# Kernel optimization log

Hardware: AMD Instinct MI355X
Metric: run time of the kernel (lower is better)

Reference implementation:

```python
import jax, jax.numpy as jnp
import numpy as np

# RWKV6Attention config (fla): expand_k=expand_v=0.5, proj_low_rank_dim=64, gate_low_rank_dim=64
H = 2048          # hidden_size
NH = 16           # num heads
KD = H // 2       # key_dim = hidden * expand_k
VD = H // 2       # value_dim = hidden * expand_v
DK = KD // NH     # head_qk_dim = 64
DV = VD // NH     # head_v_dim = 64
RLOW = 64         # proj_low_rank_dim
GLOW = 64         # gate_low_rank_dim
EPS = 1e-5
B, T = 2, 1024


def setup_inputs() -> dict:
    key = jax.random.key(0)
    ks = jax.random.split(key, 18)

    def rn(k, shape, scale=0.02):
        return (jax.random.normal(k, shape) * scale).astype(jnp.float32)

    return {
        "x": jax.random.normal(ks[0], (B, T, H), dtype=jnp.float32),
        "mu_x": rn(ks[1], (H,), 0.5),            # LerpLinear mixing coeff
        "Wx1": rn(ks[2], (H, 5 * RLOW)),          # x_proj[0].linear (hidden -> 5*r)
        "Wx2": rn(ks[3], (H, 5, RLOW)),           # x_proj[2].weight viewed [hidden, 5, r]
        "x_bias": rn(ks[4], (5, H)),
        "Wr": rn(ks[5], (H, KD)),
        "Wk": rn(ks[6], (H, KD)),
        "Wv": rn(ks[7], (H, VD)),
        "Ww_a": rn(ks[8], (H, GLOW)),             # w_proj LoRA down
        "Ww_b": rn(ks[9], (GLOW, KD)),            # w_proj LoRA up
        "bw": rn(ks[10], (KD,)),
        "Wg_a": rn(ks[11], (H, GLOW)),            # g_proj LoRA down
        "Wg_b": rn(ks[12], (GLOW, VD)),           # g_proj LoRA up
        "bg": rn(ks[13], (VD,)),
        "bonus": rn(ks[14], (NH, DK), 0.5),       # per-head bonus u
        "ln_w": jnp.ones((DV,), jnp.float32),     # FusedLayerNormSwishGate affine
        "ln_b": jnp.zeros((DV,), jnp.float32),
        "Wo": rn(ks[15], (VD, H)),
    }


def reference(x, mu_x, Wx1, Wx2, x_bias, Wr, Wk, Wv, Ww_a, Ww_b, bw,
              Wg_a, Wg_b, bg, bonus, ln_w, ln_b, Wo):
    b, t, _ = x.shape
    # time_shift: zero-pad one step at front, drop last
    shifted = jnp.pad(x, ((0, 0), (1, 0), (0, 0)))[:, :t]
    delta = shifted - x

    # low-rank data-dependent lerp coefficients for r, w, k, v, g
    lr = jnp.tanh(((x + delta * mu_x) @ Wx1).reshape(b, t, 5, RLOW))
    mus = jnp.einsum('btnr,hnr->btnh', lr, Wx2) + x_bias  # [B,T,5,H]
    mr, mw, mk, mv, mg = (mus[:, :, i] for i in range(5))

    r = (x + delta * mr) @ Wr                                   # [B,T,KD]
    w = jnp.tanh((x + delta * mw) @ Ww_a) @ Ww_b + bw           # [B,T,KD]
    k = (x + delta * mk) @ Wk                                   # [B,T,KD]
    v = (x + delta * mv) @ Wv                                   # [B,T,VD]
    g = jnp.tanh((x + delta * mg) @ Wg_a) @ Wg_b + bg           # [B,T,VD]

    r = r.reshape(b, t, NH, DK)
    k = k.reshape(b, t, NH, DK)
    v = v.reshape(b, t, NH, DV)
    decay = jnp.exp(-jnp.exp(w.reshape(b, t, NH, DK)))          # w = -exp(w); decay = exp(w)

    # linear-attention recurrence: o_t = r_t . (S + u * k_t v_t^T); S <- decay_t * S + k_t v_t^T
    xs = (jnp.moveaxis(r, 1, 0), jnp.moveaxis(k, 1, 0),
          jnp.moveaxis(v, 1, 0), jnp.moveaxis(decay, 1, 0))
    S0 = jnp.zeros((b, NH, DK, DV), x.dtype)

    def step(S, inp):
        rt, kt, vt, dt = inp
        kv = kt[..., :, None] * vt[..., None, :]                # [B,NH,DK,DV]
        ot = jnp.einsum('bhk,bhkv->bhv', rt, S + bonus[None, :, :, None] * kv)
        S = dt[..., None] * S + kv
        return S, ot

    _, o = jax.lax.scan(step, S0, xs)                           # o: [T,B,NH,DV]
    o = jnp.moveaxis(o, 0, 1)                                   # [B,T,NH,DV]

    # per-head layernorm + swish gate
    g = g.reshape(b, t, NH, DV)
    mean = o.mean(-1, keepdims=True)
    var = o.var(-1, keepdims=True)
    on = (o - mean) * jax.lax.rsqrt(var + EPS) * ln_w + ln_b
    o = on * g * jax.nn.sigmoid(g)

    return o.reshape(b, t, VD) @ Wo
```

## Files before the change

### kernel.cpp

```cpp
#include <hip/hip_runtime.h>
#include <hip/hip_bf16.h>

#define H_    2048
#define NH_   16
#define KD_   1024
#define DK_   64
#define T_    1024
#define B_    2
#define M_    (B_*T_)
#define RL_   64
#define CC_   32
#define NC_   (T_/CC_)

typedef short bf16x8 __attribute__((ext_vector_type(8)));
typedef float f32x4  __attribute__((ext_vector_type(4)));

__device__ __forceinline__ ushort bf16r(float f) {
    union { float f; unsigned u; } v; v.f = f;
    return (ushort)((v.u + 0x7FFF + ((v.u >> 16) & 1)) >> 16);
}

__device__ __forceinline__ void gl_lds16(const void* g, void* l) {
    __builtin_amdgcn_global_load_lds((const __attribute__((address_space(1))) void*)g,
                                     (__attribute__((address_space(3))) void*)l, 16, 0, 0);
}


__global__ __launch_bounds__(256) void mix_mu_t(const float* __restrict__ x,
                                                const float* __restrict__ mu,
                                                ushort* __restrict__ At) {
    int c = blockIdx.x * 256 + threadIdx.x;
    int bt = c >> 8, k8 = c & 255;
    int k = k8 << 3;
    int t = bt & (T_ - 1);
    const float* xp = &x[(size_t)bt * H_ + k];
    float4 xa = *(const float4*)xp;
    float4 xb = *(const float4*)(xp + 4);
    float4 sa = make_float4(0,0,0,0), sb = make_float4(0,0,0,0);
    if (t > 0) { sa = *(const float4*)(xp - H_); sb = *(const float4*)(xp - H_ + 4); }
    float4 ma = *(const float4*)&mu[k];
    float4 mb = *(const float4*)&mu[k + 4];
    ushort o[8];
    o[0] = bf16r(xa.x + (sa.x - xa.x) * ma.x);
    o[1] = bf16r(xa.y + (sa.y - xa.y) * ma.y);
    o[2] = bf16r(xa.z + (sa.z - xa.z) * ma.z);
    o[3] = bf16r(xa.w + (sa.w - xa.w) * ma.w);
    o[4] = bf16r(xb.x + (sb.x - xb.x) * mb.x);
    o[5] = bf16r(xb.y + (sb.y - xb.y) * mb.y);
    o[6] = bf16r(xb.z + (sb.z - xb.z) * mb.z);
    o[7] = bf16r(xb.w + (sb.w - xb.w) * mb.w);
    int rb = bt >> 7, kb = k8 >> 2, g = k8 & 3, r = bt & 127;
    *(uint4*)&At[(((size_t)(rb * 64 + kb)) << 12) + ((g << 7) + r) * 8] = *(uint4*)o;
}

__global__ __launch_bounds__(256) void convert_w(const float* __restrict__ W,
                                                 ushort* __restrict__ Wt,
                                                 int K, int N) {
    __shared__ float s[32][68];
    int kb = blockIdx.y, nb = blockIdx.x;
    int t = threadIdx.x;
    #pragma unroll
    for (int i = 0; i < 2; ++i) {
        int q = t + i * 256;
        int k = q >> 4, c4 = (q & 15) << 2;
        *(float4*)&s[k][c4] = *(const float4*)&W[(size_t)(kb * 32 + k) * N + nb * 64 + c4];
    }
    __syncthreads();
    int g = t >> 6, c = t & 63;
    ushort o[8];
    #pragma unroll
    for (int e = 0; e < 8; ++e) o[e] = bf16r(s[g * 8 + e][c]);
    *(uint4*)&Wt[((size_t)(nb * (K >> 5) + kb)) * 2048 + t * 8] = *(uint4*)o;
}

__global__ __launch_bounds__(256) void convert_w3(const float* __restrict__ W0,
                                                  const float* __restrict__ W1,
                                                  const float* __restrict__ W2,
                                                  ushort* __restrict__ Wt) {
    __shared__ float s[32][68];
    int z = blockIdx.z;
    const float* W = (z == 0) ? W0 : (z == 1) ? W1 : W2;
    ushort* dst = Wt + (size_t)z * ((size_t)H_ * KD_);
    int kb = blockIdx.y, nb = blockIdx.x;
    int t = threadIdx.x;
    #pragma unroll
    for (int i = 0; i < 2; ++i) {
        int q = t + i * 256;
        int k = q >> 4, c4 = (q & 15) << 2;
        *(float4*)&s[k][c4] = *(const float4*)&W[(size_t)(kb * 32 + k) * KD_ + nb * 64 + c4];
    }
    __syncthreads();
    int g = t >> 6, c = t & 63;
    ushort o[8];
    #pragma unroll
    for (int e = 0; e < 8; ++e) o[e] = bf16r(s[g * 8 + e][c]);
    *(uint4*)&dst[((size_t)(nb * (H_ >> 5) + kb)) * 2048 + t * 8] = *(uint4*)o;
}

template<int EPI, int NB>
__global__ __launch_bounds__(256) void gemm_bf16t(const ushort* __restrict__ A0,
                                                  const ushort* __restrict__ A1,
                                                  const ushort* __restrict__ A2,
                                                  const ushort* __restrict__ Bt0,
                                                  float* __restrict__ C0,
                                                  int K, int ldc) {
    __shared__ ushort Alds[2][4096];
    __shared__ ushort Blds[2][2048];
    int tid = threadIdx.x;
    int w = tid >> 6, l = tid & 63;
    int KB = K >> 5;
    int z = (NB > 1) ? blockIdx.z : 0;
    const ushort* At = (NB > 1) ? (z == 0 ? A0 : z == 1 ? A1 : A2) : A0;
    const ushort* Bt = Bt0 + (size_t)z * ((size_t)H_ * KD_);
    float* C = C0 + (size_t)z * ((size_t)M_ * KD_);
    const ushort* Ag = At + (size_t)blockIdx.y * KB * 4096 + tid * 8;
    const ushort* Bg = Bt + (size_t)blockIdx.x * KB * 2048 + tid * 8;
    int wr = (w >> 1) << 6, wc = (w & 1) << 5;
    int a_off = (((l >> 4) << 7) + wr + (l & 15)) << 3;
    int b_off = (((l >> 4) << 6) + wc + (l & 15)) << 3;
    f32x4 acc[8] = {};
    gl_lds16(Ag,        &Alds[0][w * 512]);
    gl_lds16(Ag + 2048, &Alds[0][w * 512 + 2048]);
    gl_lds16(Bg,        &Blds[0][w * 512]);
    __syncthreads();
    for (int kt = 0; kt < KB; ++kt) {
        int cur = kt & 1;
        if (kt + 1 < KB) {
            Ag += 4096; Bg += 2048;
            int nxt = cur ^ 1;
            gl_lds16(Ag,        &Alds[nxt][w * 512]);
            gl_lds16(Ag + 2048, &Alds[nxt][w * 512 + 2048]);
            gl_lds16(Bg,        &Blds[nxt][w * 512]);
        }
        bf16x8 af0 = *(const bf16x8*)&Alds[cur][a_off];
        bf16x8 af1 = *(const bf16x8*)&Alds[cur][a_off + 128];
        bf16x8 af2 = *(const bf16x8*)&Alds[cur][a_off + 256];
        bf16x8 af3 = *(const bf16x8*)&Alds[cur][a_off + 384];
        bf16x8 bf0 = *(const bf16x8*)&Blds[cur][b_off];
        bf16x8 bf1 = *(const bf16x8*)&Blds[cur][b_off + 128];
        acc[0] = __builtin_amdgcn_mfma_f32_16x16x32_bf16(af0, bf0, acc[0], 0, 0, 0);
        acc[1] = __builtin_amdgcn_mfma_f32_16x16x32_bf16(af0, bf1, acc[1], 0, 0, 0);
        acc[2] = __builtin_amdgcn_mfma_f32_16x16x32_bf16(af1, bf0, acc[2], 0, 0, 0);
        acc[3] = __builtin_amdgcn_mfma_f32_16x16x32_bf16(af1, bf1, acc[3], 0, 0, 0);
        acc[4] = __builtin_amdgcn_mfma_f32_16x16x32_bf16(af2, bf0, acc[4], 0, 0, 0);
        acc[5] = __builtin_amdgcn_mfma_f32_16x16x32_bf16(af2, bf1, acc[5], 0, 0, 0);
        acc[6] = __builtin_amdgcn_mfma_f32_16x16x32_bf16(af3, bf0, acc[6], 0, 0, 0);
        acc[7] = __builtin_amdgcn_mfma_f32_16x16x32_bf16(af3, bf1, acc[7], 0, 0, 0);
        __syncthreads();
    }
    int row0 = (blockIdx.y << 7) + wr + ((l >> 4) << 2);
    int col0 = (blockIdx.x << 6) + wc + (l & 15);
    #pragma unroll
    for (int fr = 0; fr < 4; ++fr)
        #pragma unroll
        for (int fc = 0; fc < 2; ++fc) {
            f32x4 v = acc[fr * 2 + fc];
            #pragma unroll
            for (int q = 0; q < 4; ++q) {
                float o = v[q];
                if (EPI == 1) o = tanhf(o);
                C[(size_t)(row0 + fr * 16 + q) * ldc + col0 + fc * 16] = o;
            }
        }
}

__global__ __launch_bounds__(256) void musgemm5_kernel(const float* __restrict__ x,
                                                       const float* __restrict__ lr,
                                                       const float* __restrict__ Wx2,
                                                       const float* __restrict__ xbias,
                                                       ushort* __restrict__ xmt_r,
                                                       float*  __restrict__ xm_w,
                                                       ushort* __restrict__ xmt_k,
                                                       ushort* __restrict__ xmt_v,
                                                       float*  __restrict__ xm_g) {
    __shared__ float sLT[64][68];
    __shared__ float sWT[64][68];
    int tid = threadIdx.x;
    int tx = tid & 15, ty = tid >> 4;
    int col0 = blockIdx.x * 64;
    int row0 = blockIdx.y * 64;
    int kcol = col0 + (tx << 2);
    int lrow = tid >> 2;
    int lk   = (tid & 3) << 2;
    #pragma unroll
    for (int b = 0; b < 5; ++b) {
        __syncthreads();
        #pragma unroll
        for (int pass = 0; pass < 4; ++pass) {
            int kk = lk + pass * 16;
            float4 lv = *(const float4*)&lr[(size_t)(row0 + lrow) * 320 + b * 64 + kk];
            float4 wv = *(const float4*)&Wx2[(size_t)(col0 + lrow) * 320 + b * 64 + kk];
            sLT[kk + 0][lrow] = lv.x; sLT[kk + 1][lrow] = lv.y;
            sLT[kk + 2][lrow] = lv.z; sLT[kk + 3][lrow] = lv.w;
            sWT[kk + 0][lrow] = wv.x; sWT[kk + 1][lrow] = wv.y;
            sWT[kk + 2][lrow] = wv.z; sWT[kk + 3][lrow] = wv.w;
        }
        __syncthreads();
        float acc[4][4] = {};
        #pragma unroll 4
        for (int k = 0; k < 64; ++k) {
            float4 a = *(const float4*)&sLT[k][ty << 2];
            float4 bb = *(const float4*)&sWT[k][tx << 2];
            float aa[4] = {a.x, a.y, a.z, a.w};
            float bv_[4] = {bb.x, bb.y, bb.z, bb.w};
            #pragma unroll
            for (int i = 0; i < 4; ++i)
                #pragma unroll
                for (int j = 0; j < 4; ++j)
                    acc[i][j] = fmaf(aa[i], bv_[j], acc[i][j]);
        }
        float4 bias4 = *(const float4*)&xbias[b * H_ + kcol];
        float bv[4] = {bias4.x, bias4.y, bias4.z, bias4.w};
        #pragma unroll
        for (int i = 0; i < 4; ++i) {
            int r = row0 + (ty << 2) + i;
            int t = r & (T_ - 1);
            const float* xrow = &x[(size_t)r * H_ + kcol];
            float4 xv = *(const float4*)xrow;
            float4 sh = make_float4(0.f, 0.f, 0.f, 0.f);
            if (t > 0) sh = *(const float4*)(xrow - H_);
            float o0 = xv.x + (sh.x - xv.x) * (acc[i][0] + bv[0]);
            float o1 = xv.y + (sh.y - xv.y) * (acc[i][1] + bv[1]);
            float o2 = xv.z + (sh.z - xv.z) * (acc[i][2] + bv[2]);
            float o3 = xv.w + (sh.w - xv.w) * (acc[i][3] + bv[3]);
            if (b == 0 || b == 2 || b == 3) {
                ushort* dst = (b == 0) ? xmt_r : (b == 2) ? xmt_k : xmt_v;
                int rb = r >> 7, kb = kcol >> 5, g = (kcol >> 3) & 3, hf = (kcol >> 2) & 1;
                ushort4 pk; pk.x = bf16r(o0); pk.y = bf16r(o1); pk.z = bf16r(o2); pk.w = bf16r(o3);
                *(ushort4*)&dst[(((size_t)(rb * 64 + kb)) << 12) + ((g << 7) + (r & 127)) * 8 + hf * 4] = pk;
            } else {
                float* dst = (b == 1) ? xm_w : xm_g;
                float4 o; o.x = o0; o.y = o1; o.z = o2; o.w = o3;
                *(float4*)&dst[(size_t)r * H_ + kcol] = o;
            }
        }
    }
}

__global__ __launch_bounds__(256) void gemm_f32_up2(const float* __restrict__ hidw,
                                                    const float* __restrict__ hidg,
                                                    const float* __restrict__ Wwb,
                                                    const float* __restrict__ Wgb,
                                                    const float* __restrict__ bw,
                                                    const float* __restrict__ bg,
                                                    float* __restrict__ db,
                                                    float* __restrict__ gb) {
    __shared__ float As[16][68];
    __shared__ float Bs[16][68];
    int z = blockIdx.z;
    const float* A = z ? hidg : hidw;
    const float* W = z ? Wgb : Wwb;
    const float* bias = z ? bg : bw;
    float* C = z ? gb : db;
    int tid = threadIdx.x;
    int tx = tid & 15, ty = tid >> 4;
    int row0 = blockIdx.y * 64, col0 = blockIdx.x * 64;
    int am = tid >> 2, ak = (tid & 3) << 2;
    int bk = tid >> 4, bn = (tid & 15) << 2;
    float acc[4][4] = {};
    float4 av = *(const float4*)&A[(size_t)(row0 + am) * 64 + ak];
    float4 bv = *(const float4*)&W[(size_t)bk * KD_ + col0 + bn];
    for (int k0 = 0; k0 < 64; k0 += 16) {
        __syncthreads();
        As[ak + 0][am] = av.x; As[ak + 1][am] = av.y;
        As[ak + 2][am] = av.z; As[ak + 3][am] = av.w;
        *(float4*)&Bs[bk][bn] = bv;
        __syncthreads();
        if (k0 + 16 < 64) {
            av = *(const float4*)&A[(size_t)(row0 + am) * 64 + k0 + 16 + ak];
            bv = *(const float4*)&W[(size_t)(k0 + 16 + bk) * KD_ + col0 + bn];
        }
        #pragma unroll
        for (int kk = 0; kk < 16; ++kk) {
            float4 a = *(const float4*)&As[kk][ty << 2];
            float4 b = *(const float4*)&Bs[kk][tx << 2];
            float aa[4] = {a.x, a.y, a.z, a.w};
            float bb[4] = {b.x, b.y, b.z, b.w};
            #pragma unroll
            for (int i = 0; i < 4; ++i)
                #pragma unroll
                for (int j = 0; j < 4; ++j)
                    acc[i][j] = fmaf(aa[i], bb[j], acc[i][j]);
        }
    }
    #pragma unroll
    for (int i = 0; i < 4; ++i) {
        int r = row0 + (ty << 2) + i;
        #pragma unroll
        for (int j = 0; j < 4; ++j) {
            int c = col0 + (tx << 2) + j;
            float v = acc[i][j] + bias[c];
            if (z == 0) v = -expf(v);
            C[(size_t)r * KD_ + c] = v;
        }
    }
}

__global__ __launch_bounds__(256) void gemm_f32_splitk2(const float* __restrict__ Aw,
                                                        const float* __restrict__ Ag2,
                                                        const float* __restrict__ Wwa,
                                                        const float* __restrict__ Wga,
                                                        float* __restrict__ partw,
                                                        float* __restrict__ partg) {
    __shared__ float As[16][68];
    __shared__ float Bs[16][68];
    int z = blockIdx.z;
    const float* A = z ? Ag2 : Aw;
    const float* W = z ? Wga : Wwa;
    float* part = z ? partg : partw;
    int tid = threadIdx.x;
    int tx = tid & 15, ty = tid >> 4;
    int row0 = blockIdx.y * 64;
    int kbase = blockIdx.x * 256;
    int am = tid >> 2, ak = (tid & 3) << 2;
    int bk = tid >> 4, bn = (tid & 15) << 2;
    float acc[4][4] = {};
    float4 av = *(const float4*)&A[(size_t)(row0 + am) * H_ + kbase + ak];
    float4 bv = *(const float4*)&W[(size_t)(kbase + bk) * 64 + bn];
    for (int k0 = 0; k0 < 256; k0 += 16) {
        __syncthreads();
        As[ak + 0][am] = av.x; As[ak + 1][am] = av.y;
        As[ak + 2][am] = av.z; As[ak + 3][am] = av.w;
        *(float4*)&Bs[bk][bn] = bv;
        __syncthreads();
        if (k0 + 16 < 256) {
            av = *(const float4*)&A[(size_t)(row0 + am) * H_ + kbase + k0 + 16 + ak];
            bv = *(const float4*)&W[(size_t)(kbase + k0 + 16 + bk) * 64 + bn];
        }
        #pragma unroll
        for (int kk = 0; kk < 16; ++kk) {
            float4 a = *(const float4*)&As[kk][ty << 2];
            float4 b = *(const float4*)&Bs[kk][tx << 2];
            float aa[4] = {a.x, a.y, a.z, a.w};
            float bb[4] = {b.x, b.y, b.z, b.w};
            #pragma unroll
            for (int i = 0; i < 4; ++i)
                #pragma unroll
                for (int j = 0; j < 4; ++j)
                    acc[i][j] = fmaf(aa[i], bb[j], acc[i][j]);
        }
    }
    float* pc = part + (size_t)blockIdx.x * (M_ * 64);
    #pragma unroll
    for (int i = 0; i < 4; ++i) {
        int r = row0 + (ty << 2) + i;
        #pragma unroll
        for (int j = 0; j < 4; ++j)
            pc[(size_t)r * 64 + (tx << 2) + j] = acc[i][j];
    }
}

__global__ __launch_bounds__(256) void reduce_tanh2(const float* __restrict__ partw,
                                                    const float* __restrict__ partg,
                                                    float* __restrict__ hidw,
                                                    float* __restrict__ hidg) {
    int z = blockIdx.y;
    const float4* p = (const float4*)(z ? partg : partw);
    float* hid = z ? hidg : hidw;
    int i = blockIdx.x * 256 + threadIdx.x;
    float4 s = p[i];
    #pragma unroll
    for (int kc = 1; kc < 8; ++kc) {
        float4 v = p[i + kc * 32768];
        s.x += v.x; s.y += v.y; s.z += v.z; s.w += v.w;
    }
    s.x = tanhf(s.x); s.y = tanhf(s.y); s.z = tanhf(s.z); s.w = tanhf(s.w);
    ((float4*)hid)[i] = s;
}

__global__ __launch_bounds__(256) void scan_chunkA(const float* r, const float* k,
                                                   const float* v, const float* ld,
                                                   const float* u,
                                                   float* rt, float* ointra,
                                                   float* Bc, float* Dc) {
    __shared__ float sR[CC_][68], sK[CC_][68], sV[CC_][68], sW[CC_][68];
    __shared__ float wc[CC_ + 1][64];
    __shared__ float sA[CC_][36];
    __shared__ float diag[CC_];
    __shared__ float sU[64];
    int bid = blockIdx.x;
    int bh = bid >> 5, c = bid & (NC_ - 1);
    int b = bh >> 4, h = bh & 15;
    int tid = threadIdx.x;
    size_t base = ((size_t)(b * T_ + c * CC_)) * KD_ + h * 64;

    for (int q = tid; q < CC_ * 16; q += 256) {
        int row = q >> 4, col4 = (q & 15) << 2;
        size_t gi = base + (size_t)row * KD_ + col4;
        *(float4*)&sR[row][col4] = *(const float4*)&r[gi];
        *(float4*)&sK[row][col4] = *(const float4*)&k[gi];
        *(float4*)&sV[row][col4] = *(const float4*)&v[gi];
        *(float4*)&sW[row][col4] = *(const float4*)&ld[gi];
    }
    if (tid < 64) sU[tid] = u[h * 64 + tid];
    __syncthreads();

    if (tid < 64) {
        float acc = 0.f;
        wc[0][tid] = 0.f;
        #pragma unroll
        for (int s = 0; s < CC_; ++s) { acc += sW[s][tid]; wc[s + 1][tid] = acc; }
    }
    {
        int tau = tid >> 3, g = tid & 7;
        float p = 0.f;
        #pragma unroll
        for (int q = 0; q < 8; ++q) {
            int i = g * 8 + q;
            p += sR[tau][i] * sU[i] * sK[tau][i];
        }
        p += __shfl_xor(p, 1, 64); p += __shfl_xor(p, 2, 64); p += __shfl_xor(p, 4, 64);
        if (g == 0) diag[tau] = p;
    }
    __syncthreads();

    for (int q = tid; q < CC_ * 64; q += 256) {
        int s = q >> 6, i = q & 63;
        float wcs  = wc[s][i];
        float wcs1 = wc[s + 1][i];
        float wcc  = wc[CC_][i];
        float rt_ = sR[s][i] * expf(wcs);
        float kt_ = sK[s][i] * expf(-wcs1);
        float bb  = sK[s][i] * expf(wcc - wcs1);
        sR[s][i] = rt_;
        sW[s][i] = kt_;
        sK[s][i] = bb;
        rt[base + (size_t)s * KD_ + i] = rt_;
    }
    if (tid < 64) Dc[(size_t)bid * 64 + tid] = expf(wc[CC_][tid]);
    __syncthreads();

    {
        int tau = tid >> 3, s0 = (tid & 7) * 4;
        float a0 = 0, a1 = 0, a2 = 0, a3 = 0;
        for (int i0 = 0; i0 < 64; i0 += 4) {
            int i = (i0 + s0) & 63;
            float4 rr = *(const float4*)&sR[tau][i];
            float4 k0v = *(const float4*)&sW[s0 + 0][i];
            float4 k1v = *(const float4*)&sW[s0 + 1][i];
            float4 k2v = *(const float4*)&sW[s0 + 2][i];
            float4 k3v = *(const float4*)&sW[s0 + 3][i];
            a0 += rr.x * k0v.x + rr.y * k0v.y + rr.z * k0v.z + rr.w * k0v.w;
            a1 += rr.x * k1v.x + rr.y * k1v.y + rr.z * k1v.z + rr.w * k1v.w;
            a2 += rr.x * k2v.x + rr.y * k2v.y + rr.z * k2v.z + rr.w * k2v.w;
            a3 += rr.x * k3v.x + rr.y * k3v.y + rr.z * k3v.z + rr.w * k3v.w;
        }
        sA[tau][s0 + 0] = (s0 + 0 < tau) ? a0 : ((s0 + 0 == tau) ? diag[tau] : 0.f);
        sA[tau][s0 + 1] = (s0 + 1 < tau) ? a1 : ((s0 + 1 == tau) ? diag[tau] : 0.f);
        sA[tau][s0 + 2] = (s0 + 2 < tau) ? a2 : ((s0 + 2 == tau) ? diag[tau] : 0.f);
        sA[tau][s0 + 3] = (s0 + 3 < tau) ? a3 : ((s0 + 3 == tau) ? diag[tau] : 0.f);
    }
    __syncthreads();

    {
        int tau = tid >> 3, j0 = (tid & 7) * 8;
        float o_[8] __attribute__((aligned(16))) = {};
        for (int s = 0; s < CC_; ++s) {
            float a = sA[tau][s];
            #pragma unroll
            for (int q = 0; q < 8; ++q) o_[q] += a * sV[s][j0 + q];
        }
        size_t ob = base + (size_t)tau * KD_ + j0;
        *(float4*)&ointra[ob]     = *(float4*)&o_[0];
        *(float4*)&ointra[ob + 4] = *(float4*)&o_[4];
    }
    {
        int i = tid >> 2, j0 = (tid & 3) * 16;
        float bacc[16] __attribute__((aligned(16))) = {};
        for (int s = 0; s < CC_; ++s) {
            float bi = sK[s][i];
            #pragma unroll
            for (int q = 0; q < 16; ++q) bacc[q] += bi * sV[s][j0 + q];
        }
        size_t bb = ((size_t)bid << 12) + i * 64 + j0;
        *(float4*)&Bc[bb + 0]  = *(float4*)&bacc[0];
        *(float4*)&Bc[bb + 4]  = *(float4*)&bacc[4];
        *(float4*)&Bc[bb + 8]  = *(float4*)&bacc[8];
        *(float4*)&Bc[bb + 12] = *(float4*)&bacc[12];
    }
}

__global__ __launch_bounds__(256) void scan_chunkB(float* BS, const float* __restrict__ Dc) {
    int g = blockIdx.x * 256 + threadIdx.x;
    int bh = g >> 12, ij = g & 4095, i = ij >> 6;
    float S = 0.f;
    size_t base = ((size_t)bh << 17) + ij;
    float bv = BS[base];
    float d  = Dc[(size_t)(bh * NC_) * 64 + i];
    for (int c = 0; c < NC_; ++c) {
        size_t idx = base + ((size_t)c << 12);
        float bv2 = 0.f, d2 = 0.f;
        if (c + 1 < NC_) {
            bv2 = BS[idx + 4096];
            d2  = Dc[(size_t)(bh * NC_ + c + 1) * 64 + i];
        }
        BS[idx] = S;
        S = d * S + bv;
        bv = bv2; d = d2;
    }
}

__global__ __launch_bounds__(256) void scan_chunkC_ln(const float* __restrict__ rt,
                                                      const float* __restrict__ BS,
                                                      const float* __restrict__ oi,
                                                      const float* __restrict__ gb,
                                                      const float* __restrict__ lw,
                                                      const float* __restrict__ lb,
                                                      ushort* __restrict__ outt) {
    __shared__ float sS[64][64];
    __shared__ float sRt[CC_][68];
    int bid = blockIdx.x;
    int bh = bid >> 5, c = bid & (NC_ - 1);
    int b = bh >> 4, h = bh & 15;
    int tid = threadIdx.x;
    size_t sbase = ((size_t)bid) << 12;
    for (int q = tid; q < 1024; q += 256)
        *(float4*)&sS[q >> 4][(q & 15) << 2] = *(const float4*)&BS[sbase + (q << 2)];
    size_t base = ((size_t)(b * T_ + c * CC_)) * KD_ + h * 64;
    for (int q = tid; q < CC_ * 16; q += 256) {
        int row = q >> 4, col4 = (q & 15) << 2;
        *(float4*)&sRt[row][col4] = *(const float4*)&rt[base + (size_t)row * KD_ + col4];
    }
    __syncthreads();
    int tau = tid >> 3, j0 = (tid & 7) * 8;
    size_t obase = base + (size_t)tau * KD_ + j0;
    float acc[8] __attribute__((aligned(16)));
    *(float4*)&acc[0] = *(const float4*)&oi[obase];
    *(float4*)&acc[4] = *(const float4*)&oi[obase + 4];
    for (int i = 0; i < 64; ++i) {
        float a = sRt[tau][i];
        #pragma unroll
        for (int q = 0; q < 8; ++q) acc[q] += a * sS[i][j0 + q];
    }
    float s = 0.f;
    #pragma unroll
    for (int q = 0; q < 8; ++q) s += acc[q];
    s += __shfl_xor(s, 1, 64); s += __shfl_xor(s, 2, 64); s += __shfl_xor(s, 4, 64);
    float mean = s * (1.f / 64.f);
    float s2 = 0.f;
    #pragma unroll
    for (int q = 0; q < 8; ++q) { float dx = acc[q] - mean; s2 += dx * dx; }
    s2 += __shfl_xor(s2, 1, 64); s2 += __shfl_xor(s2, 2, 64); s2 += __shfl_xor(s2, 4, 64);
    float inv = rsqrtf(s2 * (1.f / 64.f) + 1e-5f);
    float4 lw0 = *(const float4*)&lw[j0], lw1 = *(const float4*)&lw[j0 + 4];
    float4 lb0 = *(const float4*)&lb[j0], lb1 = *(const float4*)&lb[j0 + 4];
    float lwv[8] = {lw0.x, lw0.y, lw0.z, lw0.w, lw1.x, lw1.y, lw1.z, lw1.w};
    float lbv[8] = {lb0.x, lb0.y, lb0.z, lb0.w, lb1.x, lb1.y, lb1.z, lb1.w};
    float4 gv0 = *(const float4*)&gb[obase], gv1 = *(const float4*)&gb[obase + 4];
    float gvv[8] = {gv0.x, gv0.y, gv0.z, gv0.w, gv1.x, gv1.y, gv1.z, gv1.w};
    ushort o8[8];
    #pragma unroll
    for (int q = 0; q < 8; ++q) {
        float on = (acc[q] - mean) * inv * lwv[q] + lbv[q];
        float gv = gvv[q];
        o8[q] = bf16r(on * gv / (1.f + expf(-gv)));
    }
    int mrow = b * T_ + c * CC_ + tau;
    int col  = h * 64 + j0;
    int rb2 = mrow >> 7, kb2 = col >> 5, gg = (col >> 3) & 3;
    *(uint4*)&outt[(((size_t)(rb2 * 32 + kb2)) << 12) + ((gg << 7) + (mrow & 127)) * 8] = *(uint4*)o8;
}

extern "C" void kernel_launch(void* const* d_in, const int* in_sizes, int n_in,
                              void* d_out, int out_size, void* d_ws, size_t ws_size,
                              hipStream_t stream) {
    const float* x     = (const float*)d_in[0];
    const float* mu_x  = (const float*)d_in[1];
    const float* Wx1   = (const float*)d_in[2];
    const float* Wx2   = (const float*)d_in[3];
    const float* xbias = (const float*)d_in[4];
    const float* Wr    = (const float*)d_in[5];
    const float* Wk    = (const float*)d_in[6];
    const float* Wv    = (const float*)d_in[7];
    const float* Ww_a  = (const float*)d_in[8];
    const float* Ww_b  = (const float*)d_in[9];
    const float* bw    = (const float*)d_in[10];
    const float* Wg_a  = (const float*)d_in[11];
    const float* Wg_b  = (const float*)d_in[12];
    const float* bg    = (const float*)d_in[13];
    const float* bonus = (const float*)d_in[14];
    const float* ln_w  = (const float*)d_in[15];
    const float* ln_b  = (const float*)d_in[16];
    const float* Wo    = (const float*)d_in[17];
    float* out = (float*)d_out;

    float* ws   = (float*)d_ws;
    float* xm   = ws;
    float* lr   = xm   + (size_t)M_ * H_;
    float* hidw = lr   + (size_t)M_ * 320;
    float* hidg = hidw + (size_t)M_ * 64;
    float* rb_  = hidg + (size_t)M_ * 64;
    float* kb_  = rb_  + (size_t)M_ * KD_;
    float* vb_  = kb_  + (size_t)M_ * KD_;
    float* db_  = vb_  + (size_t)M_ * KD_;
    float* gb_  = db_  + (size_t)M_ * KD_;
    float* ob_  = gb_  + (size_t)M_ * KD_;
    float* BS   = ob_  + (size_t)M_ * KD_;
    float* Dc   = BS   + (size_t)1024 * 4096;
    float* wend = Dc + (size_t)1024 * 64;
    ushort* xmt_r = (ushort*)xm;
    ushort* xmt_k = (ushort*)(xm + (size_t)M_ * H_ / 2);
    ushort* xmt_v = (ushort*)(BS + 1310720);
    float*  xm_w  = rb_;
    float*  xm_g  = vb_;
    float*  partw = BS;
    float*  partg = gb_;
    ushort* gt    = (ushort*)xm;
    ushort* Wx1t  = (ushort*)wend;
    ushort* Wrt   = Wx1t + (size_t)H_ * 320;
    ushort* Wkt   = Wrt  + (size_t)H_ * KD_;
    ushort* Wvt   = Wkt  + (size_t)H_ * KD_;
    ushort* Wot   = Wvt  + (size_t)H_ * KD_;

    dim3 blk(256);
    const int elems8 = M_ * H_ / 8;

    convert_w<<<dim3(320 / 64, H_ / 32), blk, 0, stream>>>(Wx1, Wx1t, H_, 320);
    convert_w3<<<dim3(KD_ / 64, H_ / 32, 3), blk, 0, stream>>>(Wr, Wk, Wv, Wrt);
    convert_w<<<dim3(H_ / 64, KD_ / 32), blk, 0, stream>>>(Wo, Wot, KD_, H_);

    mix_mu_t<<<elems8 / 256, blk, 0, stream>>>(x, mu_x, (ushort*)xm);
    gemm_bf16t<1, 1><<<dim3(320 / 64, M_ / 128), blk, 0, stream>>>((ushort*)xm, nullptr, nullptr,
                                                                   Wx1t, lr, H_, 320);

    musgemm5_kernel<<<dim3(H_ / 64, M_ / 64), blk, 0, stream>>>(x, lr, Wx2, xbias,
                                                                xmt_r, xm_w, xmt_k, xmt_v, xm_g);

    gemm_f32_splitk2<<<dim3(8, M_ / 64, 2), blk, 0, stream>>>(xm_w, xm_g, Ww_a, Wg_a,
                                                              partw, partg);
    reduce_tanh2<<<dim3(128, 2), blk, 0, stream>>>(partw, partg, hidw, hidg);

    gemm_f32_up2<<<dim3(KD_ / 64, M_ / 64, 2), blk, 0, stream>>>(hidw, hidg, Ww_b, Wg_b,
                                                                 bw, bg, db_, gb_);

    gemm_bf16t<0, 3><<<dim3(KD_ / 64, M_ / 128, 3), blk, 0, stream>>>(xmt_r, xmt_k, xmt_v,
                                                                      Wrt, rb_, H_, KD_);

    scan_chunkA<<<B_ * NH_ * NC_, blk, 0, stream>>>(rb_, kb_, vb_, db_, bonus,
                                                    rb_ , ob_, BS, Dc);
    scan_chunkB<<<(B_ * NH_ * 4096) / 256, blk, 0, stream>>>(BS, Dc);
    scan_chunkC_ln<<<B_ * NH_ * NC_, blk, 0, stream>>>(rb_, BS, ob_, gb_, ln_w, ln_b, gt);

    gemm_bf16t<0, 1><<<dim3(H_ / 64, M_ / 128), blk, 0, stream>>>(gt, nullptr, nullptr,
                                                                  Wot, out, KD_, H_);
}
```

Baseline: 276.3 us.

## Parallelize musgemm5 over the five mix branches and enlarge row tile to 128

The five-branch loop inside musgemm5_kernel becomes a grid z-dimension, so each block handles one branch. The row tile grows from 64 to 128, and each thread now computes 8x4 outputs instead of 4x4. This gives more independent blocks (2.5x) and drops the per-branch syncs, while reusing each Wx2 tile across more rows. The cost is that x and its shifted row are now re-read once per branch block instead of staying cached within one block, plus more registers and LDS per block.

```diff
diff --git a/kernel.cpp b/kernel.cpp
--- a/kernel.cpp
+++ b/kernel.cpp
@@ -173,66 +173,76 @@
                                                        ushort* __restrict__ xmt_k,
                                                        ushort* __restrict__ xmt_v,
                                                        float*  __restrict__ xm_g) {
-    __shared__ float sLT[64][68];
+    __shared__ float sLT[64][136];
     __shared__ float sWT[64][68];
     int tid = threadIdx.x;
     int tx = tid & 15, ty = tid >> 4;
+    int b = blockIdx.z;
     int col0 = blockIdx.x * 64;
-    int row0 = blockIdx.y * 64;
-    int kcol = col0 + (tx << 2);
-    int lrow = tid >> 2;
-    int lk   = (tid & 3) << 2;
-    #pragma unroll
-    for (int b = 0; b < 5; ++b) {
-        __syncthreads();
-        #pragma unroll
-        for (int pass = 0; pass < 4; ++pass) {
-            int kk = lk + pass * 16;
-            float4 lv = *(const float4*)&lr[(size_t)(row0 + lrow) * 320 + b * 64 + kk];
-            float4 wv = *(const float4*)&Wx2[(size_t)(col0 + lrow) * 320 + b * 64 + kk];
+    int row0 = blockIdx.y * 128;
+    {
+        int lrow = tid >> 1, lk = (tid & 1) << 5;
+        const float* lrp = &lr[(size_t)(row0 + lrow) * 320 + b * 64 + lk];
+        #pragma unroll
+        for (int pass = 0; pass < 8; ++pass) {
+            float4 lv = *(const float4*)(lrp + pass * 4);
+            int kk = lk + pass * 4;
             sLT[kk + 0][lrow] = lv.x; sLT[kk + 1][lrow] = lv.y;
             sLT[kk + 2][lrow] = lv.z; sLT[kk + 3][lrow] = lv.w;
-            sWT[kk + 0][lrow] = wv.x; sWT[kk + 1][lrow] = wv.y;
-            sWT[kk + 2][lrow] = wv.z; sWT[kk + 3][lrow] = wv.w;
-        }
-        __syncthreads();
-        float acc[4][4] = {};
-        #pragma unroll 4
-        for (int k = 0; k < 64; ++k) {
-            float4 a = *(const float4*)&sLT[k][ty << 2];
-            float4 bb = *(const float4*)&sWT[k][tx << 2];
-            float aa[4] = {a.x, a.y, a.z, a.w};
-            float bv_[4] = {bb.x, bb.y, bb.z, bb.w};
+        }
+    }
+    {
+        int wrow = tid >> 2, wk = (tid & 3) << 2;
+        const float* wxp = &Wx2[(size_t)(col0 + wrow) * 320 + b * 64];
+        #pragma unroll
+        for (int pass = 0; pass < 4; ++pass) {
+            int kk = wk + pass * 16;
+            float4 wv = *(const float4*)(wxp + kk);
+            sWT[kk + 0][wrow] = wv.x; sWT[kk + 1][wrow] = wv.y;
+            sWT[kk + 2][wrow] = wv.z; sWT[kk + 3][wrow] = wv.w;
+        }
+    }
+    __syncthreads();
+    int r0 = ty << 3;
+    int c0 = tx << 2;
+    int kcol = col0 + c0;
+    float acc[8][4] = {};
+    #pragma unroll 4
+    for (int k = 0; k < 64; ++k) {
+        float4 a0 = *(const float4*)&sLT[k][r0];
+        float4 a1 = *(const float4*)&sLT[k][r0 + 4];
+        float4 bb = *(const float4*)&sWT[k][c0];
+        float aa[8] = {a0.x, a0.y, a0.z, a0.w, a1.x, a1.y, a1.z, a1.w};
+        float bv_[4] = {bb.x, bb.y, bb.z, bb.w};
+        #pragma unroll
+        for (int i = 0; i < 8; ++i)
             #pragma unroll
-            for (int i = 0; i < 4; ++i)
-                #pragma unroll
-                for (int j = 0; j < 4; ++j)
-                    acc[i][j] = fmaf(aa[i], bv_[j], acc[i][j]);
-        }
-        float4 bias4 = *(const float4*)&xbias[b * H_ + kcol];
-        float bv[4] = {bias4.x, bias4.y, bias4.z, bias4.w};
-        #pragma unroll
-        for (int i = 0; i < 4; ++i) {
-            int r = row0 + (ty << 2) + i;
-            int t = r & (T_ - 1);
-            const float* xrow = &x[(size_t)r * H_ + kcol];
-            float4 xv = *(const float4*)xrow;
-            float4 sh = make_float4(0.f, 0.f, 0.f, 0.f);
-            if (t > 0) sh = *(const float4*)(xrow - H_);
-            float o0 = xv.x + (sh.x - xv.x) * (acc[i][0] + bv[0]);
-            float o1 = xv.y + (sh.y - xv.y) * (acc[i][1] + bv[1]);
-            float o2 = xv.z + (sh.z - xv.z) * (acc[i][2] + bv[2]);
-            float o3 = xv.w + (sh.w - xv.w) * (acc[i][3] + bv[3]);
-            if (b == 0 || b == 2 || b == 3) {
-                ushort* dst = (b == 0) ? xmt_r : (b == 2) ? xmt_k : xmt_v;
-                int rb = r >> 7, kb = kcol >> 5, g = (kcol >> 3) & 3, hf = (kcol >> 2) & 1;
-                ushort4 pk; pk.x = bf16r(o0); pk.y = bf16r(o1); pk.z = bf16r(o2); pk.w = bf16r(o3);
-                *(ushort4*)&dst[(((size_t)(rb * 64 + kb)) << 12) + ((g << 7) + (r & 127)) * 8 + hf * 4] = pk;
-            } else {
-                float* dst = (b == 1) ? xm_w : xm_g;
-                float4 o; o.x = o0; o.y = o1; o.z = o2; o.w = o3;
-                *(float4*)&dst[(size_t)r * H_ + kcol] = o;
-            }
+            for (int j = 0; j < 4; ++j)
+                acc[i][j] = fmaf(aa[i], bv_[j], acc[i][j]);
+    }
+    float4 bias4 = *(const float4*)&xbias[b * H_ + kcol];
+    float bv[4] = {bias4.x, bias4.y, bias4.z, bias4.w};
+    #pragma unroll
+    for (int i = 0; i < 8; ++i) {
+        int r = row0 + r0 + i;
+        int t = r & (T_ - 1);
+        const float* xrow = &x[(size_t)r * H_ + kcol];
+        float4 xv = *(const float4*)xrow;
+        float4 sh = make_float4(0.f, 0.f, 0.f, 0.f);
+        if (t > 0) sh = *(const float4*)(xrow - H_);
+        float o0 = xv.x + (sh.x - xv.x) * (acc[i][0] + bv[0]);
+        float o1 = xv.y + (sh.y - xv.y) * (acc[i][1] + bv[1]);
+        float o2 = xv.z + (sh.z - xv.z) * (acc[i][2] + bv[2]);
+        float o3 = xv.w + (sh.w - xv.w) * (acc[i][3] + bv[3]);
+        if (b == 0 || b == 2 || b == 3) {
+            ushort* dst = (b == 0) ? xmt_r : (b == 2) ? xmt_k : xmt_v;
+            int rb = r >> 7, kb = kcol >> 5, g = (kcol >> 3) & 3, hf = (kcol >> 2) & 1;
+            ushort4 pk; pk.x = bf16r(o0); pk.y = bf16r(o1); pk.z = bf16r(o2); pk.w = bf16r(o3);
+            *(ushort4*)&dst[(((size_t)(rb * 64 + kb)) << 12) + ((g << 7) + (r & 127)) * 8 + hf * 4] = pk;
+        } else {
+            float* dst = (b == 1) ? xm_w : xm_g;
+            float4 o; o.x = o0; o.y = o1; o.z = o2; o.w = o3;
+            *(float4*)&dst[(size_t)r * H_ + kcol] = o;
         }
     }
 }
@@ -623,8 +633,8 @@
     gemm_bf16t<1, 1><<<dim3(320 / 64, M_ / 128), blk, 0, stream>>>((ushort*)xm, nullptr, nullptr,
                                                                    Wx1t, lr, H_, 320);
 
-    musgemm5_kernel<<<dim3(H_ / 64, M_ / 64), blk, 0, stream>>>(x, lr, Wx2, xbias,
-                                                                xmt_r, xm_w, xmt_k, xmt_v, xm_g);
+    musgemm5_kernel<<<dim3(H_ / 64, M_ / 128, 5), blk, 0, stream>>>(x, lr, Wx2, xbias,
+                                                                    xmt_r, xm_w, xmt_k, xmt_v, xm_g);
 
     gemm_f32_splitk2<<<dim3(8, M_ / 64, 2), blk, 0, stream>>>(xm_w, xm_g, Ww_a, Wg_a,
                                                               partw, partg);
```

Measured after the change: 275.1 us. About the same (-0.4%).

## Compute LoRA mix expansion with bf16 MFMA and pre-tiled tanh output

Applied to the files above, without the earlier changes.

Replaces the fp32 FMA-based musgemm5 kernel with an MFMA bf16 kernel that expands the low-rank lerp coefficients. The Wx1 GEMM now writes tanh outputs as bf16 directly in the tiled layout the new kernel loads via global_load_lds, and Wx2 is pre-converted into a matching tiled bf16 layout. This removes the scalar fp32 inner loop and the transposed LDS staging, at the cost of bf16 precision on the mixing coefficients and scalar (non-vectorised) epilogue loads and stores of x and outputs.

```diff
diff --git a/kernel.cpp b/kernel.cpp
--- a/kernel.cpp
+++ b/kernel.cpp
@@ -97,6 +97,26 @@
     *(uint4*)&dst[((size_t)(nb * (H_ >> 5) + kb)) * 2048 + t * 8] = *(uint4*)o;
 }
 
+__global__ __launch_bounds__(256) void convert_wx2(const float* __restrict__ Wx2,
+                                                   ushort* __restrict__ Wt) {
+    __shared__ float s[64][68];
+    int nb = blockIdx.x, z = blockIdx.y;
+    int t = threadIdx.x;
+    for (int q = t; q < 1024; q += 256) {
+        int row = q >> 4, c4 = (q & 15) << 2;
+        *(float4*)&s[row][c4] = *(const float4*)&Wx2[(size_t)(nb * 64 + row) * 320 + z * 64 + c4];
+    }
+    __syncthreads();
+    for (int q = t; q < 512; q += 256) {
+        int kb = q >> 8, i = q & 255;
+        int g = i >> 6, c = i & 63;
+        ushort o[8];
+        #pragma unroll
+        for (int e = 0; e < 8; ++e) o[e] = bf16r(s[c][kb * 32 + g * 8 + e]);
+        *(uint4*)&Wt[(((size_t)(z * 32 + nb)) * 2 + kb) * 2048 + i * 8] = *(uint4*)o;
+    }
+}
+
 template<int EPI, int NB>
 __global__ __launch_bounds__(256) void gemm_bf16t(const ushort* __restrict__ A0,
                                                   const ushort* __restrict__ A1,
@@ -164,77 +184,139 @@
         }
 }
 
-__global__ __launch_bounds__(256) void musgemm5_kernel(const float* __restrict__ x,
-                                                       const float* __restrict__ lr,
-                                                       const float* __restrict__ Wx2,
-                                                       const float* __restrict__ xbias,
-                                                       ushort* __restrict__ xmt_r,
-                                                       float*  __restrict__ xm_w,
-                                                       ushort* __restrict__ xmt_k,
-                                                       ushort* __restrict__ xmt_v,
-                                                       float*  __restrict__ xm_g) {
-    __shared__ float sLT[64][68];
-    __shared__ float sWT[64][68];
+__global__ __launch_bounds__(256) void gemm_bf16t_lr(const ushort* __restrict__ At,
+                                                     const ushort* __restrict__ Bt,
+                                                     ushort* __restrict__ lrt) {
+    __shared__ ushort Alds[2][4096];
+    __shared__ ushort Blds[2][2048];
     int tid = threadIdx.x;
-    int tx = tid & 15, ty = tid >> 4;
-    int col0 = blockIdx.x * 64;
-    int row0 = blockIdx.y * 64;
-    int kcol = col0 + (tx << 2);
-    int lrow = tid >> 2;
-    int lk   = (tid & 3) << 2;
-    #pragma unroll
-    for (int b = 0; b < 5; ++b) {
+    int w = tid >> 6, l = tid & 63;
+    const int KB = H_ >> 5;
+    const ushort* Ag = At + (size_t)blockIdx.y * KB * 4096 + tid * 8;
+    const ushort* Bg = Bt + (size_t)blockIdx.x * KB * 2048 + tid * 8;
+    int wr = (w >> 1) << 6, wc = (w & 1) << 5;
+    int a_off = (((l >> 4) << 7) + wr + (l & 15)) << 3;
+    int b_off = (((l >> 4) << 6) + wc + (l & 15)) << 3;
+    f32x4 acc[8] = {};
+    gl_lds16(Ag,        &Alds[0][w * 512]);
+    gl_lds16(Ag + 2048, &Alds[0][w * 512 + 2048]);
+    gl_lds16(Bg,        &Blds[0][w * 512]);
+    __syncthreads();
+    for (int kt = 0; kt < KB; ++kt) {
+        int cur = kt & 1;
+        if (kt + 1 < KB) {
+            Ag += 4096; Bg += 2048;
+            int nxt = cur ^ 1;
+            gl_lds16(Ag,        &Alds[nxt][w * 512]);
+            gl_lds16(Ag + 2048, &Alds[nxt][w * 512 + 2048]);
+            gl_lds16(Bg,        &Blds[nxt][w * 512]);
+        }
+        bf16x8 af0 = *(const bf16x8*)&Alds[cur][a_off];
+        bf16x8 af1 = *(const bf16x8*)&Alds[cur][a_off + 128];
+        bf16x8 af2 = *(const bf16x8*)&Alds[cur][a_off + 256];
+        bf16x8 af3 = *(const bf16x8*)&Alds[cur][a_off + 384];
+        bf16x8 bf0 = *(const bf16x8*)&Blds[cur][b_off];
+        bf16x8 bf1 = *(const bf16x8*)&Blds[cur][b_off + 128];
+        acc[0] = __builtin_amdgcn_mfma_f32_16x16x32_bf16(af0, bf0, acc[0], 0, 0, 0);
+        acc[1] = __builtin_amdgcn_mfma_f32_16x16x32_bf16(af0, bf1, acc[1], 0, 0, 0);
+        acc[2] = __builtin_amdgcn_mfma_f32_16x16x32_bf16(af1, bf0, acc[2], 0, 0, 0);
+        acc[3] = __builtin_amdgcn_mfma_f32_16x16x32_bf16(af1, bf1, acc[3], 0, 0, 0);
+        acc[4] = __builtin_amdgcn_mfma_f32_16x16x32_bf16(af2, bf0, acc[4], 0, 0, 0);
+        acc[5] = __builtin_amdgcn_mfma_f32_16x16x32_bf16(af2, bf1, acc[5], 0, 0, 0);
+        acc[6] = __builtin_amdgcn_mfma_f32_16x16x32_bf16(af3, bf0, acc[6], 0, 0, 0);
+        acc[7] = __builtin_amdgcn_mfma_f32_16x16x32_bf16(af3, bf1, acc[7], 0, 0, 0);
         __syncthreads();
-        #pragma unroll
-        for (int pass = 0; pass < 4; ++pass) {
-            int kk = lk + pass * 16;
-            float4 lv = *(const float4*)&lr[(size_t)(row0 + lrow) * 320 + b * 64 + kk];
-            float4 wv = *(const float4*)&Wx2[(size_t)(col0 + lrow) * 320 + b * 64 + kk];
-            sLT[kk + 0][lrow] = lv.x; sLT[kk + 1][lrow] = lv.y;
-            sLT[kk + 2][lrow] = lv.z; sLT[kk + 3][lrow] = lv.w;
-            sWT[kk + 0][lrow] = wv.x; sWT[kk + 1][lrow] = wv.y;
-            sWT[kk + 2][lrow] = wv.z; sWT[kk + 3][lrow] = wv.w;
-        }
-        __syncthreads();
-        float acc[4][4] = {};
-        #pragma unroll 4
-        for (int k = 0; k < 64; ++k) {
-            float4 a = *(const float4*)&sLT[k][ty << 2];
-            float4 bb = *(const float4*)&sWT[k][tx << 2];
-            float aa[4] = {a.x, a.y, a.z, a.w};
-            float bv_[4] = {bb.x, bb.y, bb.z, bb.w};
+    }
+    int rloc0 = wr + ((l >> 4) << 2);
+    size_t tbase = ((size_t)(blockIdx.y * 5 + blockIdx.x)) * 8192;
+    #pragma unroll
+    for (int fr = 0; fr < 4; ++fr)
+        #pragma unroll
+        for (int fc = 0; fc < 2; ++fc) {
+            f32x4 v = acc[fr * 2 + fc];
+            int c = wc + fc * 16 + (l & 15);
+            int kb2 = c >> 5, g = (c >> 3) & 3, e = c & 7;
             #pragma unroll
-            for (int i = 0; i < 4; ++i)
-                #pragma unroll
-                for (int j = 0; j < 4; ++j)
-                    acc[i][j] = fmaf(aa[i], bv_[j], acc[i][j]);
-        }
-        float4 bias4 = *(const float4*)&xbias[b * H_ + kcol];
-        float bv[4] = {bias4.x, bias4.y, bias4.z, bias4.w};
-        #pragma unroll
-        for (int i = 0; i < 4; ++i) {
-            int r = row0 + (ty << 2) + i;
-            int t = r & (T_ - 1);
-            const float* xrow = &x[(size_t)r * H_ + kcol];
-            float4 xv = *(const float4*)xrow;
-            float4 sh = make_float4(0.f, 0.f, 0.f, 0.f);
-            if (t > 0) sh = *(const float4*)(xrow - H_);
-            float o0 = xv.x + (sh.x - xv.x) * (acc[i][0] + bv[0]);
-            float o1 = xv.y + (sh.y - xv.y) * (acc[i][1] + bv[1]);
-            float o2 = xv.z + (sh.z - xv.z) * (acc[i][2] + bv[2]);
-            float o3 = xv.w + (sh.w - xv.w) * (acc[i][3] + bv[3]);
-            if (b == 0 || b == 2 || b == 3) {
-                ushort* dst = (b == 0) ? xmt_r : (b == 2) ? xmt_k : xmt_v;
-                int rb = r >> 7, kb = kcol >> 5, g = (kcol >> 3) & 3, hf = (kcol >> 2) & 1;
-                ushort4 pk; pk.x = bf16r(o0); pk.y = bf16r(o1); pk.z = bf16r(o2); pk.w = bf16r(o3);
-                *(ushort4*)&dst[(((size_t)(rb * 64 + kb)) << 12) + ((g << 7) + (r & 127)) * 8 + hf * 4] = pk;
-            } else {
-                float* dst = (b == 1) ? xm_w : xm_g;
-                float4 o; o.x = o0; o.y = o1; o.z = o2; o.w = o3;
-                *(float4*)&dst[(size_t)r * H_ + kcol] = o;
+            for (int q = 0; q < 4; ++q) {
+                int r = rloc0 + fr * 16 + q;
+                lrt[tbase + (size_t)kb2 * 4096 + ((g << 7) + r) * 8 + e] = bf16r(tanhf(v[q]));
             }
         }
-    }
+}
+
+__global__ __launch_bounds__(256) void musgemm_mfma(const ushort* __restrict__ lrt,
+                                                    const ushort* __restrict__ wx2t,
+                                                    const float* __restrict__ x,
+                                                    const float* __restrict__ xbias,
+                                                    ushort* __restrict__ xmt_r,
+                                                    float*  __restrict__ xm_w,
+                                                    ushort* __restrict__ xmt_k,
+                                                    ushort* __restrict__ xmt_v,
+                                                    float*  __restrict__ xm_g) {
+    __shared__ ushort Alds[8192];
+    __shared__ ushort Blds[4096];
+    int tid = threadIdx.x;
+    int w = tid >> 6, l = tid & 63;
+    int z = blockIdx.z;
+    const ushort* Ag = lrt + ((size_t)(blockIdx.y * 5 + z)) * 8192 + tid * 8;
+    const ushort* Bg = wx2t + ((size_t)(z * 32 + blockIdx.x)) * 4096 + tid * 8;
+    gl_lds16(Ag,        &Alds[w * 512]);
+    gl_lds16(Ag + 2048, &Alds[w * 512 + 2048]);
+    gl_lds16(Ag + 4096, &Alds[w * 512 + 4096]);
+    gl_lds16(Ag + 6144, &Alds[w * 512 + 6144]);
+    gl_lds16(Bg,        &Blds[w * 512]);
+    gl_lds16(Bg + 2048, &Blds[w * 512 + 2048]);
+    int wr = (w >> 1) << 6, wc = (w & 1) << 5;
+    int a_off = (((l >> 4) << 7) + wr + (l & 15)) << 3;
+    int b_off = (((l >> 4) << 6) + wc + (l & 15)) << 3;
+    f32x4 acc[8] = {};
+    __syncthreads();
+    #pragma unroll
+    for (int kb = 0; kb < 2; ++kb) {
+        const ushort* Ab = &Alds[kb * 4096 + a_off];
+        const ushort* Bb = &Blds[kb * 2048 + b_off];
+        bf16x8 af0 = *(const bf16x8*)(Ab);
+        bf16x8 af1 = *(const bf16x8*)(Ab + 128);
+        bf16x8 af2 = *(const bf16x8*)(Ab + 256);
+        bf16x8 af3 = *(const bf16x8*)(Ab + 384);
+        bf16x8 bf0 = *(const bf16x8*)(Bb);
+        bf16x8 bf1 = *(const bf16x8*)(Bb + 128);
+        acc[0] = __builtin_amdgcn_mfma_f32_16x16x32_bf16(af0, bf0, acc[0], 0, 0, 0);
+        acc[1] = __builtin_amdgcn_mfma_f32_16x16x32_bf16(af0, bf1, acc[1], 0, 0, 0);
+        acc[2] = __builtin_amdgcn_mfma_f32_16x16x32_bf16(af1, bf0, acc[2], 0, 0, 0);
+        acc[3] = __builtin_amdgcn_mfma_f32_16x16x32_bf16(af1, bf1, acc[3], 0, 0, 0);
+        acc[4] = __builtin_amdgcn_mfma_f32_16x16x32_bf16(af2, bf0, acc[4], 0, 0, 0);
+        acc[5] = __builtin_amdgcn_mfma_f32_16x16x32_bf16(af2, bf1, acc[5], 0, 0, 0);
+        acc[6] = __builtin_amdgcn_mfma_f32_16x16x32_bf16(af3, bf0, acc[6], 0, 0, 0);
+        acc[7] = __builtin_amdgcn_mfma_f32_16x16x32_bf16(af3, bf1, acc[7], 0, 0, 0);
+    }
+    int row0 = (blockIdx.y << 7) + wr + ((l >> 4) << 2);
+    int col0 = (blockIdx.x << 6) + wc + (l & 15);
+    #pragma unroll
+    for (int fr = 0; fr < 4; ++fr)
+        #pragma unroll
+        for (int fc = 0; fc < 2; ++fc) {
+            f32x4 v = acc[fr * 2 + fc];
+            int h = col0 + fc * 16;
+            float bias = xbias[z * H_ + h];
+            #pragma unroll
+            for (int q = 0; q < 4; ++q) {
+                int r = row0 + fr * 16 + q;
+                int t = r & (T_ - 1);
+                const float* xp = &x[(size_t)r * H_ + h];
+                float xv = *xp;
+                float sh = (t > 0) ? *(xp - H_) : 0.f;
+                float o = xv + (sh - xv) * (v[q] + bias);
+                if (z == 0 || z == 2 || z == 3) {
+                    ushort* dst = (z == 0) ? xmt_r : (z == 2) ? xmt_k : xmt_v;
+                    int rb = r >> 7, kb = h >> 5, g = (h >> 3) & 3;
+                    dst[(((size_t)(rb * 64 + kb)) << 12) + ((g << 7) + (r & 127)) * 8 + (h & 7)] = bf16r(o);
+                } else {
+                    float* dst = (z == 1) ? xm_w : xm_g;
+                    dst[(size_t)r * H_ + h] = o;
+                }
+            }
+        }
 }
 
 __global__ __launch_bounds__(256) void gemm_f32_up2(const float* __restrict__ hidw,
@@ -606,6 +688,8 @@
     float*  partw = BS;
     float*  partg = gb_;
     ushort* gt    = (ushort*)xm;
+    ushort* lrt   = (ushort*)lr;
+    ushort* wx2t  = lrt + 655360;
     ushort* Wx1t  = (ushort*)wend;
     ushort* Wrt   = Wx1t + (size_t)H_ * 320;
     ushort* Wkt   = Wrt  + (size_t)H_ * KD_;
@@ -618,13 +702,13 @@
     convert_w<<<dim3(320 / 64, H_ / 32), blk, 0, stream>>>(Wx1, Wx1t, H_, 320);
     convert_w3<<<dim3(KD_ / 64, H_ / 32, 3), blk, 0, stream>>>(Wr, Wk, Wv, Wrt);
     convert_w<<<dim3(H_ / 64, KD_ / 32), blk, 0, stream>>>(Wo, Wot, KD_, H_);
+    convert_wx2<<<dim3(32, 5), blk, 0, stream>>>(Wx2, wx2t);
 
     mix_mu_t<<<elems8 / 256, blk, 0, stream>>>(x, mu_x, (ushort*)xm);
-    gemm_bf16t<1, 1><<<dim3(320 / 64, M_ / 128), blk, 0, stream>>>((ushort*)xm, nullptr, nullptr,
-                                                                   Wx1t, lr, H_, 320);
-
-    musgemm5_kernel<<<dim3(H_ / 64, M_ / 64), blk, 0, stream>>>(x, lr, Wx2, xbias,
-                                                                xmt_r, xm_w, xmt_k, xmt_v, xm_g);
+    gemm_bf16t_lr<<<dim3(5, M_ / 128), blk, 0, stream>>>((ushort*)xm, Wx1t, lrt);
+
+    musgemm_mfma<<<dim3(H_ / 64, M_ / 128, 5), blk, 0, stream>>>(lrt, wx2t, x, xbias,
+                                                                 xmt_r, xm_w, xmt_k, xmt_v, xm_g);
 
     gemm_f32_splitk2<<<dim3(8, M_ / 64, 2), blk, 0, stream>>>(xm_w, xm_g, Ww_a, Wg_a,
                                                               partw, partg);
```

After: 266.3 us. 3.6% less time.
